# Performance work log

Measured on AMD Instinct MI355X. Metric: run time of the kernel, lower is better.

The kernel has to match this reference:

```python
import jax, jax.numpy as jnp
import numpy as np


def _gcn_layer(x, W, b, src, dst, n_dst):
    """DGL GraphConv with norm='both': D_dst^{-1/2} A D_src^{-1/2} X W + b."""
    n_src = x.shape[0]
    ones = jnp.ones(src.shape[0], dtype=x.dtype)
    out_deg = jnp.clip(jax.ops.segment_sum(ones, src, num_segments=n_src), 1.0)
    in_deg = jnp.clip(jax.ops.segment_sum(ones, dst, num_segments=n_dst), 1.0)
    xn = x * (out_deg ** -0.5)[:, None]          # [n_src, F] source-side norm
    agg = jax.ops.segment_sum(xn[src], dst, num_segments=n_dst)  # sparse SpMM
    agg = agg * (in_deg ** -0.5)[:, None]        # dest-side norm
    return agg @ W + b


def setup_inputs() -> dict:
    key = jax.random.key(0)
    ks = jax.random.split(key, 9)
    N0, N1, N2 = 200000, 100000, 50000
    E1, E2 = 1600000, 800000
    F_in, F_hid, F_out = 128, 256, 128
    x = jax.random.normal(ks[0], (N0, F_in), dtype=jnp.float32)
    src1 = jax.random.randint(ks[1], (E1,), 0, N0, dtype=jnp.int32)
    dst1 = jax.random.randint(ks[2], (E1,), 0, N1, dtype=jnp.int32)
    src2 = jax.random.randint(ks[3], (E2,), 0, N1, dtype=jnp.int32)
    dst2 = jax.random.randint(ks[4], (E2,), 0, N2, dtype=jnp.int32)
    # Glorot-uniform weights like dgl GraphConv reset_parameters
    lim1 = (6.0 / (F_in + F_hid)) ** 0.5
    lim2 = (6.0 / (F_hid + F_out)) ** 0.5
    W1 = jax.random.uniform(ks[5], (F_in, F_hid), jnp.float32, -lim1, lim1)
    b1 = jnp.zeros((F_hid,), jnp.float32)
    W2 = jax.random.uniform(ks[6], (F_hid, F_out), jnp.float32, -lim2, lim2)
    b2 = jnp.zeros((F_out,), jnp.float32)
    return {"x": x, "W1": W1, "b1": b1, "W2": W2, "b2": b2,
            "src1": src1, "dst1": dst1, "src2": src2, "dst2": dst2,
            "n_dst1": N1, "n_dst2": N2}


def reference(x, W1, b1, W2, b2, src1, dst1, src2, dst2, n_dst1, n_dst2):
    h = jax.nn.relu(_gcn_layer(x, W1, b1, src1, dst1, n_dst1))
    out = jax.nn.relu(_gcn_layer(h, W2, b2, src2, dst2, n_dst2))
    return out
```

## Files before the change

### kernel.cpp

```cpp
#include <hip/hip_runtime.h>
#include <hip/hip_bf16.h>

#define F1 128
#define F2 256
#define F3 128
#define CAP 64

#define NB1D 391
#define NB2D 196
#define NB1S 782
#define NB2S 391
#define CAPD 4608
#define CAPS 2432
#define GD1 0
#define GD2 391
#define GS1 587
#define GS2 1369

typedef __attribute__((ext_vector_type(8))) short bf16x8;
typedef __attribute__((ext_vector_type(4))) float f32x4;
typedef __attribute__((ext_vector_type(4))) unsigned int u32x4;

__device__ inline float bf2f(unsigned short u) {
    return __uint_as_float(((unsigned int)u) << 16);
}
__device__ inline unsigned short f2bf(float f) {
    __hip_bfloat16 b = __float2bfloat16(f);
    return *reinterpret_cast<unsigned short*>(&b);
}
__device__ inline unsigned int pack2(float lo, float hi) {
    return ((unsigned int)f2bf(hi) << 16) | f2bf(lo);
}

#define ACC_ROW(u, c)                                   \
    acc[0] = fmaf(c, bf2f(u.x & 0xffff), acc[0]);       \
    acc[1] = fmaf(c, bf2f(u.x >> 16), acc[1]);          \
    acc[2] = fmaf(c, bf2f(u.y & 0xffff), acc[2]);       \
    acc[3] = fmaf(c, bf2f(u.y >> 16), acc[3]);          \
    acc[4] = fmaf(c, bf2f(u.z & 0xffff), acc[4]);       \
    acc[5] = fmaf(c, bf2f(u.z >> 16), acc[5]);          \
    acc[6] = fmaf(c, bf2f(u.w & 0xffff), acc[6]);       \
    acc[7] = fmaf(c, bf2f(u.w >> 16), acc[7]);

__global__ __launch_bounds__(1024) void scatter_build(
    const int* __restrict__ src1, const int* __restrict__ dst1,
    const int* __restrict__ src2, const int* __restrict__ dst2,
    const float* __restrict__ x, const float* __restrict__ W1,
    const float* __restrict__ W2, int* __restrict__ gcnt,
    unsigned int* __restrict__ bkt_d1, unsigned int* __restrict__ bkt_d2,
    unsigned char* __restrict__ bkt_s1, unsigned char* __restrict__ bkt_s2,
    unsigned int* __restrict__ xn, unsigned short* __restrict__ Bp1,
    unsigned short* __restrict__ Bp2, int E1, int E2, int A1, int A2, int B3) {
    __shared__ int hist[1184];
    int b = blockIdx.x, t = threadIdx.x;

    if (b < A1 + A2) {
        const int L1 = (b < A1);
        const int* __restrict__ src = L1 ? src1 : src2;
        const int* __restrict__ dst = L1 ? dst1 : dst2;
        const int E = L1 ? E1 : E2;
        const int NBd = L1 ? NB1D : NB2D;
        const int NBs = L1 ? NB1S : NB2S;
        int* gd = gcnt + (L1 ? GD1 : GD2);
        int* gs = gcnt + (L1 ? GS1 : GS2);
        unsigned int* bd = L1 ? bkt_d1 : bkt_d2;
        unsigned char* bs = L1 ? bkt_s1 : bkt_s2;
        int* hd = hist;
        int* hs = hist + NBd;
        for (int i = t; i < NBd + NBs; i += 1024) hist[i] = 0;
        __syncthreads();
        int e0 = (L1 ? b : b - A1) * 8192;
        int se[8], de[8];
#pragma unroll
        for (int i = 0; i < 8; ++i) {
            int e = e0 + i * 1024 + t;
            se[i] = -1;
            de[i] = -1;
            if (e < E) {
                int s = src[e], d = dst[e];
                se[i] = s;
                de[i] = d;
                atomicAdd(&hd[d >> 8], 1);
                atomicAdd(&hs[s >> 8], 1);
            }
        }
        __syncthreads();
        for (int i = t; i < NBd; i += 1024) {
            int c = hd[i];
            hd[i] = c ? atomicAdd(&gd[i], c) : 0;
        }
        for (int i = t; i < NBs; i += 1024) {
            int c = hs[i];
            hs[i] = c ? atomicAdd(&gs[i], c) : 0;
        }
        __syncthreads();
#pragma unroll
        for (int i = 0; i < 8; ++i) {
            if (de[i] >= 0) {
                int s = se[i], d = de[i];
                int pd = atomicAdd(&hd[d >> 8], 1);
                if (pd < CAPD)
                    bd[(size_t)(d >> 8) * CAPD + pd] = ((unsigned int)s << 8) | (d & 255);
                int ps = atomicAdd(&hs[s >> 8], 1);
                if (ps < CAPS)
                    bs[(size_t)(s >> 8) * CAPS + ps] = (unsigned char)(s & 255);
            }
        }
    } else if (b < A1 + A2 + B3) {
        size_t tid = (size_t)(b - A1 - A2) * 1024 + t;
        const f32x4* xp = (const f32x4*)x;
        f32x4 a = __builtin_nontemporal_load(xp + tid * 2);
        f32x4 c = __builtin_nontemporal_load(xp + tid * 2 + 1);
        u32x4 o;
        o.x = pack2(a.x, a.y);
        o.y = pack2(a.z, a.w);
        o.z = pack2(c.x, c.y);
        o.w = pack2(c.z, c.w);
        ((u32x4*)xn)[tid] = o;
    } else {
        int w = b - (A1 + A2 + B3);
        int which = w >> 5;
        const float* W = which ? W2 : W1;
        unsigned short* out = which ? Bp2 : Bp1;
        int N = which ? F3 : F2;
        int idx = (w & 31) * 1024 + t;
        int k = idx / N, n = idx % N;
        unsigned short v = f2bf(W[idx]);
        int kt = k >> 5, q = (k >> 3) & 3, j = k & 7;
        int nt = n >> 4, lane = q * 16 + (n & 15);
        int NT = N >> 4;
        out[(((kt * NT + nt) * 64 + lane) << 3) + j] = v;
    }
}

__global__ __launch_bounds__(256) void bucket_build(
    const int* __restrict__ gcnt,
    const unsigned int* __restrict__ bkt_d1, const unsigned int* __restrict__ bkt_d2,
    const unsigned char* __restrict__ bkt_s1, const unsigned char* __restrict__ bkt_s2,
    int* __restrict__ csr1, int* __restrict__ cnt_in1, float* __restrict__ rs_in1,
    int* __restrict__ csr2, int* __restrict__ cnt_in2, float* __restrict__ rs_in2,
    float* __restrict__ rs_out1, float* __restrict__ rs_out2) {
    __shared__ int hist[256];
    int b = blockIdx.x, t = threadIdx.x;
    hist[t] = 0;
    __syncthreads();

    if (b < NB1D + NB2D) {
        const int L1 = (b < NB1D);
        int bb = L1 ? b : b - NB1D;
        const unsigned int* bkt = L1 ? bkt_d1 : bkt_d2;
        int* csr = L1 ? csr1 : csr2;
        int* cnt_in = L1 ? cnt_in1 : cnt_in2;
        float* rs_in = L1 ? rs_in1 : rs_in2;
        int Nd = L1 ? 100000 : 50000;
        int n = gcnt[(L1 ? GD1 : GD2) + bb];
        if (n > CAPD) n = CAPD;
        size_t base = (size_t)bb * CAPD;
        for (int i = t; i < n; i += 256) {
            unsigned int v = bkt[base + i];
            int d = v & 255, s = (int)(v >> 8);
            int pos = atomicAdd(&hist[d], 1);
            if (pos < CAP) csr[((size_t)(bb * 256 + d)) * CAP + pos] = s;
        }
        __syncthreads();
        int node = bb * 256 + t;
        if (node < Nd) {
            int c = hist[t];
            cnt_in[node] = c < CAP ? c : CAP;
            rs_in[node] = rsqrtf((float)(c < 1 ? 1 : c));
        }
    } else {
        const int L1 = (b < NB1D + NB2D + NB1S);
        int bb = L1 ? b - (NB1D + NB2D) : b - (NB1D + NB2D + NB1S);
        const unsigned char* bkt = L1 ? bkt_s1 : bkt_s2;
        float* rs_out = L1 ? rs_out1 : rs_out2;
        int Ns = L1 ? 200000 : 100000;
        int n = gcnt[(L1 ? GS1 : GS2) + bb];
        if (n > CAPS) n = CAPS;
        size_t base = (size_t)bb * CAPS;
        for (int i = t; i < n; i += 256) atomicAdd(&hist[bkt[base + i]], 1);
        __syncthreads();
        int node = bb * 256 + t;
        if (node < Ns) rs_out[node] = rsqrtf((float)(hist[t] < 1 ? 1 : hist[t]));
    }
}

__global__ __launch_bounds__(256) void agg128_kernel(
    const unsigned int* __restrict__ X, const int* __restrict__ csr,
    const int* __restrict__ cnt, const float* __restrict__ rs_src,
    unsigned int* __restrict__ out, int ndst) {
    int wave = (int)((blockIdx.x * blockDim.x + threadIdx.x) >> 6);
    int lane = threadIdx.x & 63;
    if (wave >= ndst) return;
    size_t base = (size_t)wave * CAP;
    int len = cnt[wave];
    int sl = 0;
    float clv = 0.f;
    if (lane < len) {
        sl = csr[base + lane];
        clv = rs_src[sl];
    }
    int eg = lane >> 4, fs = lane & 15;
    float acc[8];
#pragma unroll
    for (int i = 0; i < 8; ++i) acc[i] = 0.f;
    for (int j = 0; j < len; j += 16) {
        int jA = j + eg, jB = j + 4 + eg, jC = j + 8 + eg, jD = j + 12 + eg;
        int sA = __shfl(sl, jA);
        int sB = __shfl(sl, jB);
        int sC = __shfl(sl, jC);
        int sD = __shfl(sl, jD);
        float cA = __shfl(clv, jA);
        float cB = __shfl(clv, jB);
        float cC = __shfl(clv, jC);
        float cD = __shfl(clv, jD);
        u32x4 uA = *(const u32x4*)(X + (size_t)sA * 64 + (fs << 2));
        u32x4 uB = *(const u32x4*)(X + (size_t)sB * 64 + (fs << 2));
        u32x4 uC = *(const u32x4*)(X + (size_t)sC * 64 + (fs << 2));
        u32x4 uD = *(const u32x4*)(X + (size_t)sD * 64 + (fs << 2));
        ACC_ROW(uA, cA)
        ACC_ROW(uB, cB)
        ACC_ROW(uC, cC)
        ACC_ROW(uD, cD)
    }
#pragma unroll
    for (int i = 0; i < 8; ++i) {
        acc[i] += __shfl_xor(acc[i], 16);
        acc[i] += __shfl_xor(acc[i], 32);
    }
    if (eg == 0) {
        u32x4 o;
        o.x = pack2(acc[0], acc[1]);
        o.y = pack2(acc[2], acc[3]);
        o.z = pack2(acc[4], acc[5]);
        o.w = pack2(acc[6], acc[7]);
        *((u32x4*)(out + (size_t)wave * 64) + fs) = o;
    }
}

__global__ __launch_bounds__(512) void gemm12(
    const unsigned short* __restrict__ A,
    const unsigned short* __restrict__ Bp1,
    const unsigned short* __restrict__ Bp2,
    const float* __restrict__ rs1, const float* __restrict__ rs2,
    const float* __restrict__ bias1,
    unsigned short* __restrict__ Y, int M) {
    __shared__ unsigned short Bs[32768];
    __shared__ unsigned short tmp[128][264];
    int lane = threadIdx.x & 63, wid = threadIdx.x >> 6;
    int t = threadIdx.x;
    int row0 = blockIdx.x * 128 + wid * 16;
    int q = lane >> 4, col = lane & 15;

#pragma unroll
    for (int i = 0; i < 8; ++i)
        ((u32x4*)Bs)[i * 512 + t] = ((const u32x4*)Bp1)[i * 512 + t];
    __syncthreads();

    int mload = row0 + col;
    if (mload > M - 1) mload = M - 1;
    const unsigned short* Arow = A + (size_t)mload * F1 + q * 8;
    f32x4 acc[16];
#pragma unroll
    for (int i = 0; i < 16; ++i) acc[i] = (f32x4){0.f, 0.f, 0.f, 0.f};
#pragma unroll
    for (int kt = 0; kt < 4; ++kt) {
        bf16x8 a = *(const bf16x8*)(Arow + kt * 32);
#pragma unroll
        for (int nt = 0; nt < 16; ++nt) {
            bf16x8 b = *(const bf16x8*)(Bs + (((kt * 16 + nt) * 64 + lane) << 3));
            acc[nt] = __builtin_amdgcn_mfma_f32_16x16x32_bf16(a, b, acc[nt], 0, 0, 0);
        }
    }
#pragma unroll
    for (int r = 0; r < 4; ++r) {
        int lrow = wid * 16 + q * 4 + r;
        int m = row0 + q * 4 + r;
        int mc = m < M ? m : M - 1;
        float s1 = rs1[mc], s2 = rs2[mc];
#pragma unroll
        for (int nt = 0; nt < 16; ++nt) {
            float v = fmaxf(fmaf(acc[nt][r], s1, bias1[nt * 16 + col]), 0.f) * s2;
            tmp[lrow][nt * 16 + col] = f2bf(v);
        }
    }
    __syncthreads();

#pragma unroll
    for (int i = 0; i < 8; ++i)
        ((u32x4*)Bs)[i * 512 + t] = ((const u32x4*)Bp2)[i * 512 + t];
    __syncthreads();

    f32x4 acc2[8];
#pragma unroll
    for (int i = 0; i < 8; ++i) acc2[i] = (f32x4){0.f, 0.f, 0.f, 0.f};
    const unsigned short* trow = &tmp[wid * 16 + col][q * 8];
#pragma unroll
    for (int kt = 0; kt < 8; ++kt) {
        bf16x8 a = *(const bf16x8*)(trow + kt * 32);
#pragma unroll
        for (int nt = 0; nt < 8; ++nt) {
            bf16x8 b = *(const bf16x8*)(Bs + (((kt * 8 + nt) * 64 + lane) << 3));
            acc2[nt] = __builtin_amdgcn_mfma_f32_16x16x32_bf16(a, b, acc2[nt], 0, 0, 0);
        }
    }
#pragma unroll
    for (int r = 0; r < 4; ++r) {
        int m = row0 + q * 4 + r;
        if (m >= M) continue;
#pragma unroll
        for (int nt = 0; nt < 8; ++nt)
            Y[(size_t)m * F3 + nt * 16 + col] = f2bf(acc2[nt][r]);
    }
}

__global__ __launch_bounds__(256) void agg_final(
    const unsigned int* __restrict__ Yv, const int* __restrict__ csr,
    const int* __restrict__ cnt, const float* __restrict__ rs_dst,
    const float* __restrict__ b2, float* __restrict__ out, int ndst) {
    int wave = (int)((blockIdx.x * blockDim.x + threadIdx.x) >> 6);
    int lane = threadIdx.x & 63;
    if (wave >= ndst) return;
    size_t base = (size_t)wave * CAP;
    int len = cnt[wave];
    int sl = 0;
    float clv = 0.f;
    if (lane < len) {
        sl = csr[base + lane];
        clv = 1.f;
    }
    int eg = lane >> 4, fs = lane & 15;
    float acc[8];
#pragma unroll
    for (int i = 0; i < 8; ++i) acc[i] = 0.f;
    for (int j = 0; j < len; j += 16) {
        int jA = j + eg, jB = j + 4 + eg, jC = j + 8 + eg, jD = j + 12 + eg;
        int sA = __shfl(sl, jA);
        int sB = __shfl(sl, jB);
        int sC = __shfl(sl, jC);
        int sD = __shfl(sl, jD);
        float cA = __shfl(clv, jA);
        float cB = __shfl(clv, jB);
        float cC = __shfl(clv, jC);
        float cD = __shfl(clv, jD);
        u32x4 uA = *(const u32x4*)(Yv + (size_t)sA * 64 + (fs << 2));
        u32x4 uB = *(const u32x4*)(Yv + (size_t)sB * 64 + (fs << 2));
        u32x4 uC = *(const u32x4*)(Yv + (size_t)sC * 64 + (fs << 2));
        u32x4 uD = *(const u32x4*)(Yv + (size_t)sD * 64 + (fs << 2));
        ACC_ROW(uA, cA)
        ACC_ROW(uB, cB)
        ACC_ROW(uC, cC)
        ACC_ROW(uD, cD)
    }
#pragma unroll
    for (int i = 0; i < 8; ++i) {
        acc[i] += __shfl_xor(acc[i], 16);
        acc[i] += __shfl_xor(acc[i], 32);
    }
    if (eg < 2) {
        float sc = rs_dst[wave];
        f32x4 bias = ((const f32x4*)b2)[(fs << 1) | eg];
        float v0 = eg ? acc[4] : acc[0];
        float v1 = eg ? acc[5] : acc[1];
        float v2 = eg ? acc[6] : acc[2];
        float v3 = eg ? acc[7] : acc[3];
        f32x4 o;
        o.x = fmaxf(fmaf(v0, sc, bias.x), 0.f);
        o.y = fmaxf(fmaf(v1, sc, bias.y), 0.f);
        o.z = fmaxf(fmaf(v2, sc, bias.z), 0.f);
        o.w = fmaxf(fmaf(v3, sc, bias.w), 0.f);
        __builtin_nontemporal_store(o, (f32x4*)out + (size_t)wave * 32 + (fs << 1) + eg);
    }
}

extern "C" void kernel_launch(void* const* d_in, const int* in_sizes, int n_in,
                              void* d_out, int out_size, void* d_ws, size_t ws_size,
                              hipStream_t stream) {
    const float* x  = (const float*)d_in[0];
    const float* W1 = (const float*)d_in[1];
    const float* b1 = (const float*)d_in[2];
    const float* W2 = (const float*)d_in[3];
    const float* b2 = (const float*)d_in[4];
    const int* src1 = (const int*)d_in[5];
    const int* dst1 = (const int*)d_in[6];
    const int* src2 = (const int*)d_in[7];
    const int* dst2 = (const int*)d_in[8];
    const int E1 = in_sizes[5], E2 = in_sizes[7];
    const int N0 = in_sizes[0] / F1;
    const int N1 = 100000, N2 = 50000;

    char* p = (char*)d_ws;
    int* gcnt = (int*)p; p += 2048 * 4;
    float* rs_out1 = (float*)p; p += (size_t)N0 * 4;
    float* rs_in1  = (float*)p; p += (size_t)N1 * 4;
    float* rs_out2 = (float*)p; p += (size_t)N1 * 4;
    float* rs_in2  = (float*)p; p += (size_t)N2 * 4;
    int* cnt_in1 = (int*)p; p += (size_t)N1 * 4;
    int* cnt_in2 = (int*)p; p += (size_t)N2 * 4;
    unsigned int* bkt_d1 = (unsigned int*)p; p += (size_t)NB1D * CAPD * 4;
    unsigned int* bkt_d2 = (unsigned int*)p; p += (size_t)NB2D * CAPD * 4;
    unsigned char* bkt_s1 = (unsigned char*)p; p += (size_t)NB1S * CAPS;
    unsigned char* bkt_s2 = (unsigned char*)p; p += (size_t)NB2S * CAPS;
    int* csr1 = (int*)p; p += (size_t)N1 * CAP * 4;
    int* csr2 = (int*)p; p += (size_t)N2 * CAP * 4;
    unsigned short* Bp1 = (unsigned short*)p; p += (size_t)F1 * F2 * 2;
    unsigned short* Bp2 = (unsigned short*)p; p += (size_t)F2 * F3 * 2;
    unsigned short* xn  = (unsigned short*)p; p += (size_t)N0 * F1 * 2;
    unsigned short* agg = (unsigned short*)p; p += (size_t)N1 * F1 * 2;
    unsigned short* y = xn;

    (void)hipMemsetAsync(gcnt, 0, 2048 * 4, stream);

    int A1 = (E1 + 8191) / 8192;
    int A2 = (E2 + 8191) / 8192;
    int B3 = N0 * F1 / 8 / 1024;
    scatter_build<<<A1 + A2 + B3 + 64, 1024, 0, stream>>>(
        src1, dst1, src2, dst2, x, W1, W2, gcnt,
        bkt_d1, bkt_d2, bkt_s1, bkt_s2,
        (unsigned int*)xn, Bp1, Bp2, E1, E2, A1, A2, B3);

    bucket_build<<<NB1D + NB2D + NB1S + NB2S, 256, 0, stream>>>(
        gcnt, bkt_d1, bkt_d2, bkt_s1, bkt_s2,
        csr1, cnt_in1, rs_in1, csr2, cnt_in2, rs_in2, rs_out1, rs_out2);

    agg128_kernel<<<(N1 + 3) / 4, 256, 0, stream>>>((const unsigned int*)xn, csr1,
                                                    cnt_in1, rs_out1,
                                                    (unsigned int*)agg, N1);

    gemm12<<<(N1 + 127) / 128, 512, 0, stream>>>(agg, Bp1, Bp2, rs_in1, rs_out2, b1, y, N1);

    agg_final<<<(N2 + 3) / 4, 256, 0, stream>>>((const unsigned int*)y, csr2, cnt_in2,
                                                rs_in2, b2, (float*)d_out, N2);
}
```

Before: 363.0 us.

## Stage bucket scatter in LDS, widen bucket_build blocks, use zero-row padding in agg_final

scatter_build now does a per-block counting sort in shared memory for destination and source buckets, then writes each bucket's entries contiguously to global memory. The aim is to replace scattered global stores with coalesced ones. bucket_build moves to 512 threads per block. agg_final drops the per-edge coefficient shuffles and sends inactive lanes to a zero-padded row of Y, which gemm12 now writes for rows beyond M. The trade-offs are much larger LDS use (about 60KB) and many more barriers from the serial scan, both of which can lower occupancy.

```diff
diff --git a/kernel.cpp b/kernel.cpp
--- a/kernel.cpp
+++ b/kernel.cpp
@@ -17,6 +17,8 @@
 #define GS1 587
 #define GS2 1369
 
+#define YPAD 100096
+
 typedef __attribute__((ext_vector_type(8))) short bf16x8;
 typedef __attribute__((ext_vector_type(4))) float f32x4;
 typedef __attribute__((ext_vector_type(4))) unsigned int u32x4;
@@ -42,6 +44,16 @@
     acc[6] = fmaf(c, bf2f(u.w & 0xffff), acc[6]);       \
     acc[7] = fmaf(c, bf2f(u.w >> 16), acc[7]);
 
+#define ACC_ROW_ADD(u)                          \
+    acc[0] += bf2f(u.x & 0xffff);               \
+    acc[1] += bf2f(u.x >> 16);                  \
+    acc[2] += bf2f(u.y & 0xffff);               \
+    acc[3] += bf2f(u.y >> 16);                  \
+    acc[4] += bf2f(u.z & 0xffff);               \
+    acc[5] += bf2f(u.z >> 16);                  \
+    acc[6] += bf2f(u.w & 0xffff);               \
+    acc[7] += bf2f(u.w >> 16);
+
 __global__ __launch_bounds__(1024) void scatter_build(
     const int* __restrict__ src1, const int* __restrict__ dst1,
     const int* __restrict__ src2, const int* __restrict__ dst2,
@@ -51,7 +63,10 @@
     unsigned char* __restrict__ bkt_s1, unsigned char* __restrict__ bkt_s2,
     unsigned int* __restrict__ xn, unsigned short* __restrict__ Bp1,
     unsigned short* __restrict__ Bp2, int E1, int E2, int A1, int A2, int B3) {
-    __shared__ int hist[1184];
+    __shared__ int hist[800];
+    __shared__ int scanA[800], scanB[800];
+    __shared__ unsigned int stg[8192];
+    __shared__ unsigned short bmap[8192];
     int b = blockIdx.x, t = threadIdx.x;
 
     if (b < A1 + A2) {
@@ -65,45 +80,109 @@
         int* gs = gcnt + (L1 ? GS1 : GS2);
         unsigned int* bd = L1 ? bkt_d1 : bkt_d2;
         unsigned char* bs = L1 ? bkt_s1 : bkt_s2;
-        int* hd = hist;
-        int* hs = hist + NBd;
-        for (int i = t; i < NBd + NBs; i += 1024) hist[i] = 0;
-        __syncthreads();
         int e0 = (L1 ? b : b - A1) * 8192;
         int se[8], de[8];
 #pragma unroll
-        for (int i = 0; i < 8; ++i) {
-            int e = e0 + i * 1024 + t;
-            se[i] = -1;
-            de[i] = -1;
+        for (int k = 0; k < 8; ++k) {
+            int e = e0 + k * 1024 + t;
+            se[k] = -1;
+            de[k] = -1;
             if (e < E) {
-                int s = src[e], d = dst[e];
-                se[i] = s;
-                de[i] = d;
-                atomicAdd(&hd[d >> 8], 1);
-                atomicAdd(&hs[s >> 8], 1);
-            }
-        }
-        __syncthreads();
-        for (int i = t; i < NBd; i += 1024) {
-            int c = hd[i];
-            hd[i] = c ? atomicAdd(&gd[i], c) : 0;
-        }
-        for (int i = t; i < NBs; i += 1024) {
-            int c = hs[i];
-            hs[i] = c ? atomicAdd(&gs[i], c) : 0;
-        }
-        __syncthreads();
-#pragma unroll
-        for (int i = 0; i < 8; ++i) {
-            if (de[i] >= 0) {
-                int s = se[i], d = de[i];
-                int pd = atomicAdd(&hd[d >> 8], 1);
-                if (pd < CAPD)
-                    bd[(size_t)(d >> 8) * CAPD + pd] = ((unsigned int)s << 8) | (d & 255);
-                int ps = atomicAdd(&hs[s >> 8], 1);
-                if (ps < CAPS)
-                    bs[(size_t)(s >> 8) * CAPS + ps] = (unsigned char)(s & 255);
+                se[k] = src[e];
+                de[k] = dst[e];
+            }
+        }
+
+        for (int i = t; i < NBd; i += 1024) hist[i] = 0;
+        __syncthreads();
+#pragma unroll
+        for (int k = 0; k < 8; ++k)
+            if (de[k] >= 0) atomicAdd(&hist[de[k] >> 8], 1);
+        __syncthreads();
+        {
+            int* sa = scanA;
+            int* sb = scanB;
+            for (int i = t; i < NBd; i += 1024) sa[i] = hist[i];
+            __syncthreads();
+            for (int off = 1; off < NBd; off <<= 1) {
+                for (int i = t; i < NBd; i += 1024) {
+                    int v = sa[i];
+                    if (i >= off) v += sa[i - off];
+                    sb[i] = v;
+                }
+                __syncthreads();
+                int* tp = sa; sa = sb; sb = tp;
+            }
+            for (int i = t; i < NBd; i += 1024) sb[i] = sa[i] - hist[i];
+            __syncthreads();
+#pragma unroll
+            for (int k = 0; k < 8; ++k) {
+                if (de[k] >= 0) {
+                    int bk = de[k] >> 8;
+                    int p = atomicAdd(&sb[bk], 1);
+                    stg[p] = ((unsigned int)se[k] << 8) | (de[k] & 255);
+                    bmap[p] = (unsigned short)bk;
+                }
+            }
+            __syncthreads();
+            for (int i = t; i < NBd; i += 1024) {
+                int c = hist[i];
+                int g = c ? atomicAdd(&gd[i], c) : 0;
+                sb[i] = g - (sa[i] - c);
+            }
+            __syncthreads();
+            int total = sa[NBd - 1];
+            for (int i = t; i < total; i += 1024) {
+                int bk = bmap[i];
+                int gpos = sb[bk] + i;
+                if (gpos < CAPD) bd[(size_t)bk * CAPD + gpos] = stg[i];
+            }
+        }
+        __syncthreads();
+
+        for (int i = t; i < NBs; i += 1024) hist[i] = 0;
+        __syncthreads();
+#pragma unroll
+        for (int k = 0; k < 8; ++k)
+            if (se[k] >= 0) atomicAdd(&hist[se[k] >> 8], 1);
+        __syncthreads();
+        {
+            int* sa = scanA;
+            int* sb = scanB;
+            for (int i = t; i < NBs; i += 1024) sa[i] = hist[i];
+            __syncthreads();
+            for (int off = 1; off < NBs; off <<= 1) {
+                for (int i = t; i < NBs; i += 1024) {
+                    int v = sa[i];
+                    if (i >= off) v += sa[i - off];
+                    sb[i] = v;
+                }
+                __syncthreads();
+                int* tp = sa; sa = sb; sb = tp;
+            }
+            for (int i = t; i < NBs; i += 1024) sb[i] = sa[i] - hist[i];
+            __syncthreads();
+#pragma unroll
+            for (int k = 0; k < 8; ++k) {
+                if (se[k] >= 0) {
+                    int bk = se[k] >> 8;
+                    int p = atomicAdd(&sb[bk], 1);
+                    stg[p] = (unsigned int)(se[k] & 255);
+                    bmap[p] = (unsigned short)bk;
+                }
+            }
+            __syncthreads();
+            for (int i = t; i < NBs; i += 1024) {
+                int c = hist[i];
+                int g = c ? atomicAdd(&gs[i], c) : 0;
+                sb[i] = g - (sa[i] - c);
+            }
+            __syncthreads();
+            int total = sa[NBs - 1];
+            for (int i = t; i < total; i += 1024) {
+                int bk = bmap[i];
+                int gpos = sb[bk] + i;
+                if (gpos < CAPS) bs[(size_t)bk * CAPS + gpos] = (unsigned char)stg[i];
             }
         }
     } else if (b < A1 + A2 + B3) {
@@ -133,7 +212,7 @@
     }
 }
 
-__global__ __launch_bounds__(256) void bucket_build(
+__global__ __launch_bounds__(512) void bucket_build(
     const int* __restrict__ gcnt,
     const unsigned int* __restrict__ bkt_d1, const unsigned int* __restrict__ bkt_d2,
     const unsigned char* __restrict__ bkt_s1, const unsigned char* __restrict__ bkt_s2,
@@ -142,7 +221,7 @@
     float* __restrict__ rs_out1, float* __restrict__ rs_out2) {
     __shared__ int hist[256];
     int b = blockIdx.x, t = threadIdx.x;
-    hist[t] = 0;
+    if (t < 256) hist[t] = 0;
     __syncthreads();
 
     if (b < NB1D + NB2D) {
@@ -156,7 +235,7 @@
         int n = gcnt[(L1 ? GD1 : GD2) + bb];
         if (n > CAPD) n = CAPD;
         size_t base = (size_t)bb * CAPD;
-        for (int i = t; i < n; i += 256) {
+        for (int i = t; i < n; i += 512) {
             unsigned int v = bkt[base + i];
             int d = v & 255, s = (int)(v >> 8);
             int pos = atomicAdd(&hist[d], 1);
@@ -164,7 +243,7 @@
         }
         __syncthreads();
         int node = bb * 256 + t;
-        if (node < Nd) {
+        if (t < 256 && node < Nd) {
             int c = hist[t];
             cnt_in[node] = c < CAP ? c : CAP;
             rs_in[node] = rsqrtf((float)(c < 1 ? 1 : c));
@@ -178,10 +257,10 @@
         int n = gcnt[(L1 ? GS1 : GS2) + bb];
         if (n > CAPS) n = CAPS;
         size_t base = (size_t)bb * CAPS;
-        for (int i = t; i < n; i += 256) atomicAdd(&hist[bkt[base + i]], 1);
+        for (int i = t; i < n; i += 512) atomicAdd(&hist[bkt[base + i]], 1);
         __syncthreads();
         int node = bb * 256 + t;
-        if (node < Ns) rs_out[node] = rsqrtf((float)(hist[t] < 1 ? 1 : hist[t]));
+        if (t < 256 && node < Ns) rs_out[node] = rsqrtf((float)(hist[t] < 1 ? 1 : hist[t]));
     }
 }
 
@@ -268,8 +347,8 @@
         bf16x8 a = *(const bf16x8*)(Arow + kt * 32);
 #pragma unroll
         for (int nt = 0; nt < 16; ++nt) {
-            bf16x8 b = *(const bf16x8*)(Bs + (((kt * 16 + nt) * 64 + lane) << 3));
-            acc[nt] = __builtin_amdgcn_mfma_f32_16x16x32_bf16(a, b, acc[nt], 0, 0, 0);
+            bf16x8 bfr = *(const bf16x8*)(Bs + (((kt * 16 + nt) * 64 + lane) << 3));
+            acc[nt] = __builtin_amdgcn_mfma_f32_16x16x32_bf16(a, bfr, acc[nt], 0, 0, 0);
         }
     }
 #pragma unroll
@@ -300,35 +379,31 @@
         bf16x8 a = *(const bf16x8*)(trow + kt * 32);
 #pragma unroll
         for (int nt = 0; nt < 8; ++nt) {
-            bf16x8 b = *(const bf16x8*)(Bs + (((kt * 8 + nt) * 64 + lane) << 3));
-            acc2[nt] = __builtin_amdgcn_mfma_f32_16x16x32_bf16(a, b, acc2[nt], 0, 0, 0);
+            bf16x8 bfr = *(const bf16x8*)(Bs + (((kt * 8 + nt) * 64 + lane) << 3));
+            acc2[nt] = __builtin_amdgcn_mfma_f32_16x16x32_bf16(a, bfr, acc2[nt], 0, 0, 0);
         }
     }
 #pragma unroll
     for (int r = 0; r < 4; ++r) {
         int m = row0 + q * 4 + r;
-        if (m >= M) continue;
+        int live = m < M;
 #pragma unroll
         for (int nt = 0; nt < 8; ++nt)
-            Y[(size_t)m * F3 + nt * 16 + col] = f2bf(acc2[nt][r]);
+            Y[(size_t)m * F3 + nt * 16 + col] = live ? f2bf(acc2[nt][r]) : (unsigned short)0;
     }
 }
 
 __global__ __launch_bounds__(256) void agg_final(
     const unsigned int* __restrict__ Yv, const int* __restrict__ csr,
     const int* __restrict__ cnt, const float* __restrict__ rs_dst,
-    const float* __restrict__ b2, float* __restrict__ out, int ndst) {
+    const float* __restrict__ b2, float* __restrict__ out, int ndst, int zrow) {
     int wave = (int)((blockIdx.x * blockDim.x + threadIdx.x) >> 6);
     int lane = threadIdx.x & 63;
     if (wave >= ndst) return;
     size_t base = (size_t)wave * CAP;
     int len = cnt[wave];
-    int sl = 0;
-    float clv = 0.f;
-    if (lane < len) {
-        sl = csr[base + lane];
-        clv = 1.f;
-    }
+    int sl = zrow;
+    if (lane < len) sl = csr[base + lane];
     int eg = lane >> 4, fs = lane & 15;
     float acc[8];
 #pragma unroll
@@ -339,18 +414,14 @@
         int sB = __shfl(sl, jB);
         int sC = __shfl(sl, jC);
         int sD = __shfl(sl, jD);
-        float cA = __shfl(clv, jA);
-        float cB = __shfl(clv, jB);
-        float cC = __shfl(clv, jC);
-        float cD = __shfl(clv, jD);
         u32x4 uA = *(const u32x4*)(Yv + (size_t)sA * 64 + (fs << 2));
         u32x4 uB = *(const u32x4*)(Yv + (size_t)sB * 64 + (fs << 2));
         u32x4 uC = *(const u32x4*)(Yv + (size_t)sC * 64 + (fs << 2));
         u32x4 uD = *(const u32x4*)(Yv + (size_t)sD * 64 + (fs << 2));
-        ACC_ROW(uA, cA)
-        ACC_ROW(uB, cB)
-        ACC_ROW(uC, cC)
-        ACC_ROW(uD, cD)
+        ACC_ROW_ADD(uA)
+        ACC_ROW_ADD(uB)
+        ACC_ROW_ADD(uC)
+        ACC_ROW_ADD(uD)
     }
 #pragma unroll
     for (int i = 0; i < 8; ++i) {
@@ -419,7 +490,7 @@
         bkt_d1, bkt_d2, bkt_s1, bkt_s2,
         (unsigned int*)xn, Bp1, Bp2, E1, E2, A1, A2, B3);
 
-    bucket_build<<<NB1D + NB2D + NB1S + NB2S, 256, 0, stream>>>(
+    bucket_build<<<NB1D + NB2D + NB1S + NB2S, 512, 0, stream>>>(
         gcnt, bkt_d1, bkt_d2, bkt_s1, bkt_s2,
         csr1, cnt_in1, rs_in1, csr2, cnt_in2, rs_in2, rs_out1, rs_out2);
 
@@ -430,5 +501,5 @@
     gemm12<<<(N1 + 127) / 128, 512, 0, stream>>>(agg, Bp1, Bp2, rs_in1, rs_out2, b1, y, N1);
 
     agg_final<<<(N2 + 3) / 4, 256, 0, stream>>>((const unsigned int*)y, csr2, cnt_in2,
-                                                rs_in2, b2, (float*)d_out, N2);
-}
+                                                rs_in2, b2, (float*)d_out, N2, N1);
+}
```

Result: faster. 349.3 us (-3.8%).
